# Kernel optimization log

Measured on AMD Instinct MI355X. Metric: run time of the kernel, lower is better.

The kernel has to match this reference:

```python
import jax, jax.numpy as jnp
import numpy as np


def setup_inputs() -> dict:
    key = jax.random.key(0)
    B, L, H, D = 8, 1024, 16, 64
    total_N = B * L
    qkv = jax.random.normal(key, (total_N, 3, H, D), dtype=jnp.float32)
    cu_seqlens = (jnp.arange(B + 1) * L).astype(jnp.int32)  # [B+1] cumulative lengths
    return {"qkv": qkv, "cu_seqlens": cu_seqlens, "max_seqlen": L}


def reference(qkv, cu_seqlens, max_seqlen):
    # qkv: [total_N, 3, H, D]; cu_seqlens: [B+1] int32
    total_N, _, H, D = qkv.shape
    scale = float(D) ** -0.5  # default softmax_scale = 1/sqrt(D)
    q, k, v = qkv[:, 0], qkv[:, 1], qkv[:, 2]  # each [total_N, H, D]

    starts = cu_seqlens[:-1]  # [B]
    ends = cu_seqlens[1:]     # [B]
    # Gather each ragged sequence into a padded [B, L, H, D] layout.
    pos = starts[:, None] + jnp.arange(max_seqlen, dtype=cu_seqlens.dtype)  # [B, L]
    valid = pos < ends[:, None]                                            # [B, L]
    idx = jnp.minimum(pos, total_N - 1)
    qp = q[idx]  # [B, L, H, D]
    kp = k[idx]
    vp = v[idx]

    # Per-sequence non-causal attention, softmax over keys of the same sequence.
    scores = jnp.einsum('bqhd,bkhd->bhqk', qp, kp) * scale  # [B, H, L, L]
    scores = jnp.where(valid[:, None, None, :], scores, jnp.float32(-1e30))
    attn = jax.nn.softmax(scores, axis=-1)
    outp = jnp.einsum('bhqk,bkhd->bqhd', attn, vp)  # [B, L, H, D]
    outp = outp * valid[:, :, None, None].astype(outp.dtype)  # zero padded queries

    # Scatter back to packed layout (invalid slots contribute zeros).
    out = jnp.zeros((total_N, H, D), dtype=qkv.dtype)
    out = out.at[idx.reshape(-1)].add(outp.reshape(-1, H, D))
    return out
```

## Files before the change

kernel.cpp:

```cpp
#include <hip/hip_runtime.h>


typedef __attribute__((ext_vector_type(4))) float f32x4;
typedef __attribute__((ext_vector_type(16))) float f32x16;
typedef __attribute__((ext_vector_type(8))) __bf16 bf16x8;
typedef __attribute__((ext_vector_type(8))) unsigned short us8;

#if __has_builtin(__builtin_amdgcn_exp2f)
#define EXP2F __builtin_amdgcn_exp2f
#else
#define EXP2F exp2f
#endif
#if __has_builtin(__builtin_amdgcn_rcpf)
#define RCPF __builtin_amdgcn_rcpf
#else
#define RCPF(x) (1.0f / (x))
#endif

__device__ __forceinline__ unsigned pk_bf16(float a, float b) {
#if __has_builtin(__builtin_amdgcn_cvt_pk_bf16_f32)
  auto r = __builtin_amdgcn_cvt_pk_bf16_f32(a, b);
  return __builtin_bit_cast(unsigned, r);
#else
  unsigned ra = __builtin_bit_cast(unsigned, a) + 0x8000u;
  unsigned rb = __builtin_bit_cast(unsigned, b) + 0x8000u;
  return __builtin_amdgcn_perm(rb, ra, 0x07060302u);
#endif
}

#define KSTR 72
#define BUFUS (128 * KSTR)
#define KO(b) ((b) * BUFUS)
#define VO(b) ((b) * BUFUS + 64 * KSTR)

#define BAR() asm volatile("s_waitcnt lgkmcnt(0)\n\ts_barrier" ::: "memory")

#define ISSUE(KT)                                                             \
  do {                                                                        \
    const int kb_ = (KT) * 64;                                                \
    int kt_ = s0 + kb_ + krow;                                                \
    kt_ = kt_ > tmax ? tmax : kt_;                                            \
    const float* kp_ = qkv + (size_t)kt_ * 3072 + 1024 + h64 + kd8;           \
    k0 = *(const float4*)kp_;                                                 \
    k1 = *(const float4*)(kp_ + 4);                                           \
    _Pragma("unroll") for (int cc_ = 0; cc_ < 2; ++cc_) {                     \
      _Pragma("unroll") for (int t_ = 0; t_ < 4; ++t_) {                      \
        int vt_ = s0 + kb_ + vk0 + cc_ * 4 + t_;                              \
        vt_ = vt_ > tmax ? tmax : vt_;                                        \
        vv[cc_][t_] = qkv[(size_t)vt_ * 3072 + 2048 + h64 + lane];            \
      }                                                                       \
    }                                                                         \
  } while (0)

#define COMMIT(BI)                                                            \
  do {                                                                        \
    uint4 kw_ = {pk_bf16(k0.x, k0.y), pk_bf16(k0.z, k0.w),                    \
                 pk_bf16(k1.x, k1.y), pk_bf16(k1.z, k1.w)};                   \
    *(uint4*)&smem[KO(BI) + krow * KSTR + kd8] = kw_;                         \
    _Pragma("unroll") for (int cc_ = 0; cc_ < 2; ++cc_) {                     \
      uint2 vw_ = {pk_bf16(vv[cc_][0], vv[cc_][1]),                           \
                   pk_bf16(vv[cc_][2], vv[cc_][3])};                          \
      *(uint2*)&smem[VO(BI) + lane * KSTR + vk0 + cc_ * 4] = vw_;             \
    }                                                                         \
  } while (0)

__launch_bounds__(512, 4)
__global__ void vla_fa_kernel(const float* __restrict__ qkv,
                              const int* __restrict__ cu,
                              float* __restrict__ out,
                              int B, int nflat) {
  __shared__ __align__(16) unsigned short smem[2 * BUFUS];
  __shared__ __align__(16) float ldsL[256];
  const int tid = threadIdx.x;
  const int wave = tid >> 6, lane = tid & 63;
  const int q5 = lane & 31, hi = lane >> 5;
  const int krow = tid >> 3, kd8 = (tid & 7) * 8;
  const int vk0 = wave * 8;
  const int BH = B * 16;

  for (int flat = blockIdx.x; flat < nflat; flat += gridDim.x) {
    const int b = flat % B;
    const int h = (flat / B) & 15;
    const int qb = flat / BH;
    const int s0 = cu[b], s1 = cu[b + 1];
    const int len = s1 - s0;
    if (qb * 256 >= len) continue;
    const int tmax = s1 - 1;
    const int h64 = h * 64;
    const int nkt = (len + 63) >> 6;

    float4 k0, k1;
    float vv[2][4];
    ISSUE(0);

    const float fs = 0.18033688011112042f;
    int qtok = s0 + qb * 256 + wave * 32 + q5;
    qtok = qtok > tmax ? tmax : qtok;
    const float* qp = qkv + (size_t)qtok * 3072 + h64 + hi * 8;
    bf16x8 qf[4];
#pragma unroll
    for (int ks = 0; ks < 4; ++ks) {
      float4 a = *(const float4*)(qp + ks * 16);
      float4 c = *(const float4*)(qp + ks * 16 + 4);
      uint4 w = {pk_bf16(a.x * fs, a.y * fs), pk_bf16(a.z * fs, a.w * fs),
                 pk_bf16(c.x * fs, c.y * fs), pk_bf16(c.z * fs, c.w * fs)};
      qf[ks] = __builtin_bit_cast(bf16x8, w);
    }

    f32x16 Oc[2];
#pragma unroll
    for (int dt = 0; dt < 2; ++dt)
#pragma unroll
      for (int i = 0; i < 16; ++i) Oc[dt][i] = 0.f;
    float lacc[4] = {0.f, 0.f, 0.f, 0.f};

    COMMIT(0);
    if (nkt > 1) ISSUE(1);
    BAR();

    for (int kt = 0; kt < nkt; ++kt) {
      const int cur = kt & 1;
      const int kbase = kt * 64;
      const bool partial = (len - kbase) < 64;
      bf16x8 paf[4];

#pragma unroll
      for (int t = 0; t < 2; ++t) {
        f32x16 S;
#pragma unroll
        for (int i = 0; i < 16; ++i) S[i] = 0.f;
        const int krd = KO(cur) + (t * 32 + q5) * KSTR + hi * 8;
        __builtin_amdgcn_s_setprio(1);
#pragma unroll
        for (int ks = 0; ks < 4; ++ks) {
          bf16x8 kf =
              __builtin_bit_cast(bf16x8, *(const us8*)&smem[krd + ks * 16]);
          S = __builtin_amdgcn_mfma_f32_32x32x16_bf16(kf, qf[ks], S, 0, 0, 0);
        }
        __builtin_amdgcn_s_setprio(0);
        if (partial) {
#pragma unroll
          for (int r = 0; r < 16; ++r) {
            const int key = t * 32 + (r & 3) + ((r >> 2) << 3) + hi * 4;
            if (kbase + key >= len) S[r] = -1e30f;
          }
        }
        float p[16];
#pragma unroll
        for (int r = 0; r < 16; ++r) p[r] = EXP2F(S[r]);
#pragma unroll
        for (int r = 0; r < 16; ++r) lacc[r & 3] += p[r];
#pragma unroll
        for (int m = 0; m < 2; ++m) {
          unsigned w0 = pk_bf16(p[m * 8 + 0], p[m * 8 + 1]);
          unsigned w1 = pk_bf16(p[m * 8 + 2], p[m * 8 + 3]);
          unsigned w2 = pk_bf16(p[m * 8 + 4], p[m * 8 + 5]);
          unsigned w3 = pk_bf16(p[m * 8 + 6], p[m * 8 + 7]);
          asm("v_permlane32_swap_b32 %0, %1" : "+v"(w0), "+v"(w2));
          asm("v_permlane32_swap_b32 %0, %1" : "+v"(w1), "+v"(w3));
          uint4 fw = {w0, w1, w2, w3};
          paf[t * 2 + m] = __builtin_bit_cast(bf16x8, fw);
        }
      }

      if (kt + 1 < nkt) {
        COMMIT(cur ^ 1);
        if (kt + 2 < nkt) ISSUE(kt + 2);
      }

      __builtin_amdgcn_s_setprio(1);
#pragma unroll
      for (int dt = 0; dt < 2; ++dt) {
        const int vrd = VO(cur) + (dt * 32 + q5) * KSTR + hi * 8;
#pragma unroll
        for (int kc = 0; kc < 4; ++kc) {
          bf16x8 vf =
              __builtin_bit_cast(bf16x8, *(const us8*)&smem[vrd + kc * 16]);
          Oc[dt] =
              __builtin_amdgcn_mfma_f32_32x32x16_bf16(paf[kc], vf, Oc[dt], 0, 0, 0);
        }
      }
      __builtin_amdgcn_s_setprio(0);
      BAR();
    }

    float lt = (lacc[0] + lacc[1]) + (lacc[2] + lacc[3]);
    lt += __shfl_xor(lt, 32, 64);
    if (hi == 0) ldsL[wave * 32 + q5] = lt;
    asm volatile("s_waitcnt lgkmcnt(0)" ::: "memory");
    const int rbase = qb * 256 + wave * 32;
#pragma unroll
    for (int g = 0; g < 4; ++g) {
      f32x4 lv = *(const f32x4*)&ldsL[wave * 32 + g * 8 + hi * 4];
#pragma unroll
      for (int j = 0; j < 4; ++j) {
        const int r = g * 4 + j;
        const int row = rbase + g * 8 + hi * 4 + j;
        if (row < len) {
          const float rl = RCPF(lv[j]);
          float* op = out + (size_t)(s0 + row) * 1024 + h64 + q5;
          op[0] = Oc[0][r] * rl;
          op[32] = Oc[1][r] * rl;
        }
      }
    }
  }
}

extern "C" void kernel_launch(void* const* d_in, const int* in_sizes, int n_in,
                              void* d_out, int out_size, void* d_ws, size_t ws_size,
                              hipStream_t stream) {
  const float* qkv = (const float*)d_in[0];
  const int* cu = (const int*)d_in[1];
  float* out = (float*)d_out;
  int B = in_sizes[1] - 1;
  int total_N = in_sizes[0] / (3 * 16 * 64);
  int qbmax = (total_N + 255) / 256;
  int nflat = B * 16 * qbmax;
  int nb = nflat < 512 ? nflat : 512;
  dim3 grid(nb), block(512, 1, 1);
  hipLaunchKernelGGL(vla_fa_kernel, grid, block, 0, stream, qkv, cu, out, B, nflat);
}
```

Baseline: 198.6 us.

## Software-pipeline QK^T of next tile with PV of previous tile

Restructures the key-tile loop so that each iteration issues the QK^T MFMAs for tile kt together with the PV MFMAs for tile kt-1, then does exp/pack afterwards. This lets the matrix cores overlap with the softmax exponent and bf16 packing work. It adds a prologue and epilogue and a triple-buffered V region in shared memory, which raises LDS use and register pressure from holding two score tiles plus the P fragments.

```diff
diff --git a/kernel.cpp b/kernel.cpp
--- a/kernel.cpp
+++ b/kernel.cpp
@@ -29,15 +29,15 @@
 }
 
 #define KSTR 72
-#define BUFUS (128 * KSTR)
-#define KO(b) ((b) * BUFUS)
-#define VO(b) ((b) * BUFUS + 64 * KSTR)
+#define KBUF(b) ((b) * (64 * KSTR))
+#define VBUF(b) ((2 + (b)) * (64 * KSTR))
+#define SMEM_US (5 * 64 * KSTR)
 
 #define BAR() asm volatile("s_waitcnt lgkmcnt(0)\n\ts_barrier" ::: "memory")
 
-#define ISSUE(KT)                                                             \
-  do {                                                                        \
-    const int kb_ = (KT) * 64;                                                \
+#define ISSUE(T)                                                              \
+  do {                                                                        \
+    const int kb_ = (T) * 64;                                                 \
     int kt_ = s0 + kb_ + krow;                                                \
     kt_ = kt_ > tmax ? tmax : kt_;                                            \
     const float* kp_ = qkv + (size_t)kt_ * 3072 + 1024 + h64 + kd8;           \
@@ -52,15 +52,63 @@
     }                                                                         \
   } while (0)
 
-#define COMMIT(BI)                                                            \
-  do {                                                                        \
+#define COMMIT(T)                                                             \
+  do {                                                                        \
+    const int kbi_ = (T) & 1, vbi_ = (T) % 3;                                 \
     uint4 kw_ = {pk_bf16(k0.x, k0.y), pk_bf16(k0.z, k0.w),                    \
                  pk_bf16(k1.x, k1.y), pk_bf16(k1.z, k1.w)};                   \
-    *(uint4*)&smem[KO(BI) + krow * KSTR + kd8] = kw_;                         \
+    *(uint4*)&smem[KBUF(kbi_) + krow * KSTR + kd8] = kw_;                     \
     _Pragma("unroll") for (int cc_ = 0; cc_ < 2; ++cc_) {                     \
       uint2 vw_ = {pk_bf16(vv[cc_][0], vv[cc_][1]),                           \
                    pk_bf16(vv[cc_][2], vv[cc_][3])};                          \
-      *(uint2*)&smem[VO(BI) + lane * KSTR + vk0 + cc_ * 4] = vw_;             \
+      *(uint2*)&smem[VBUF(vbi_) + lane * KSTR + vk0 + cc_ * 4] = vw_;         \
+    }                                                                         \
+  } while (0)
+
+#define QKT(SREG, TT, KB)                                                     \
+  do {                                                                        \
+    const int krd_ = KBUF(KB) + ((TT) * 32 + q5) * KSTR + hi * 8;             \
+    _Pragma("unroll") for (int ks_ = 0; ks_ < 4; ++ks_) {                     \
+      bf16x8 kf_ =                                                            \
+          __builtin_bit_cast(bf16x8, *(const us8*)&smem[krd_ + ks_ * 16]);    \
+      SREG = __builtin_amdgcn_mfma_f32_32x32x16_bf16(kf_, qf[ks_], SREG, 0,   \
+                                                     0, 0);                   \
+    }                                                                         \
+  } while (0)
+
+#define EXPPACK(SREG, TT)                                                     \
+  do {                                                                        \
+    if (partial) {                                                            \
+      _Pragma("unroll") for (int r_ = 0; r_ < 16; ++r_) {                     \
+        const int key_ = (TT) * 32 + (r_ & 3) + ((r_ >> 2) << 3) + hi * 4;    \
+        if (kbase + key_ >= len) SREG[r_] = -1e30f;                           \
+      }                                                                       \
+    }                                                                         \
+    float p_[16];                                                             \
+    _Pragma("unroll") for (int r_ = 0; r_ < 16; ++r_) p_[r_] = EXP2F(SREG[r_]); \
+    _Pragma("unroll") for (int r_ = 0; r_ < 16; ++r_) lacc[r_ & 3] += p_[r_]; \
+    _Pragma("unroll") for (int m_ = 0; m_ < 2; ++m_) {                        \
+      unsigned w0_ = pk_bf16(p_[m_ * 8 + 0], p_[m_ * 8 + 1]);                 \
+      unsigned w1_ = pk_bf16(p_[m_ * 8 + 2], p_[m_ * 8 + 3]);                 \
+      unsigned w2_ = pk_bf16(p_[m_ * 8 + 4], p_[m_ * 8 + 5]);                 \
+      unsigned w3_ = pk_bf16(p_[m_ * 8 + 6], p_[m_ * 8 + 7]);                 \
+      asm("v_permlane32_swap_b32 %0, %1" : "+v"(w0_), "+v"(w2_));             \
+      asm("v_permlane32_swap_b32 %0, %1" : "+v"(w1_), "+v"(w3_));             \
+      uint4 fw_ = {w0_, w1_, w2_, w3_};                                       \
+      paf[(TT) * 2 + m_] = __builtin_bit_cast(bf16x8, fw_);                   \
+    }                                                                         \
+  } while (0)
+
+#define PV(VB)                                                                \
+  do {                                                                        \
+    _Pragma("unroll") for (int dt_ = 0; dt_ < 2; ++dt_) {                     \
+      const int vrd_ = VBUF(VB) + (dt_ * 32 + q5) * KSTR + hi * 8;            \
+      _Pragma("unroll") for (int kc_ = 0; kc_ < 4; ++kc_) {                   \
+        bf16x8 vf_ =                                                          \
+            __builtin_bit_cast(bf16x8, *(const us8*)&smem[vrd_ + kc_ * 16]);  \
+        Oc[dt_] = __builtin_amdgcn_mfma_f32_32x32x16_bf16(paf[kc_], vf_,      \
+                                                          Oc[dt_], 0, 0, 0); \
+      }                                                                       \
     }                                                                         \
   } while (0)
 
@@ -69,7 +117,7 @@
                               const int* __restrict__ cu,
                               float* __restrict__ out,
                               int B, int nflat) {
-  __shared__ __align__(16) unsigned short smem[2 * BUFUS];
+  __shared__ __align__(16) unsigned short smem[SMEM_US];
   __shared__ __align__(16) float ldsL[256];
   const int tid = threadIdx.x;
   const int wave = tid >> 6, lane = tid & 63;
@@ -113,76 +161,56 @@
 #pragma unroll
       for (int i = 0; i < 16; ++i) Oc[dt][i] = 0.f;
     float lacc[4] = {0.f, 0.f, 0.f, 0.f};
-
+    bf16x8 paf[4];
+
+    BAR();
     COMMIT(0);
     if (nkt > 1) ISSUE(1);
     BAR();
 
-    for (int kt = 0; kt < nkt; ++kt) {
-      const int cur = kt & 1;
+    {
+      const int kbase = 0;
+      const bool partial = len < 64;
+      f32x16 S0, S1;
+#pragma unroll
+      for (int i = 0; i < 16; ++i) { S0[i] = 0.f; S1[i] = 0.f; }
+      __builtin_amdgcn_s_setprio(1);
+      QKT(S0, 0, 0);
+      QKT(S1, 1, 0);
+      __builtin_amdgcn_s_setprio(0);
+      if (nkt > 1) COMMIT(1);
+      if (nkt > 2) ISSUE(2);
+      EXPPACK(S0, 0);
+      EXPPACK(S1, 1);
+      BAR();
+    }
+
+    for (int kt = 1; kt < nkt; ++kt) {
       const int kbase = kt * 64;
       const bool partial = (len - kbase) < 64;
-      bf16x8 paf[4];
-
-#pragma unroll
-      for (int t = 0; t < 2; ++t) {
-        f32x16 S;
-#pragma unroll
-        for (int i = 0; i < 16; ++i) S[i] = 0.f;
-        const int krd = KO(cur) + (t * 32 + q5) * KSTR + hi * 8;
-        __builtin_amdgcn_s_setprio(1);
-#pragma unroll
-        for (int ks = 0; ks < 4; ++ks) {
-          bf16x8 kf =
-              __builtin_bit_cast(bf16x8, *(const us8*)&smem[krd + ks * 16]);
-          S = __builtin_amdgcn_mfma_f32_32x32x16_bf16(kf, qf[ks], S, 0, 0, 0);
-        }
-        __builtin_amdgcn_s_setprio(0);
-        if (partial) {
-#pragma unroll
-          for (int r = 0; r < 16; ++r) {
-            const int key = t * 32 + (r & 3) + ((r >> 2) << 3) + hi * 4;
-            if (kbase + key >= len) S[r] = -1e30f;
-          }
-        }
-        float p[16];
-#pragma unroll
-        for (int r = 0; r < 16; ++r) p[r] = EXP2F(S[r]);
-#pragma unroll
-        for (int r = 0; r < 16; ++r) lacc[r & 3] += p[r];
-#pragma unroll
-        for (int m = 0; m < 2; ++m) {
-          unsigned w0 = pk_bf16(p[m * 8 + 0], p[m * 8 + 1]);
-          unsigned w1 = pk_bf16(p[m * 8 + 2], p[m * 8 + 3]);
-          unsigned w2 = pk_bf16(p[m * 8 + 4], p[m * 8 + 5]);
-          unsigned w3 = pk_bf16(p[m * 8 + 6], p[m * 8 + 7]);
-          asm("v_permlane32_swap_b32 %0, %1" : "+v"(w0), "+v"(w2));
-          asm("v_permlane32_swap_b32 %0, %1" : "+v"(w1), "+v"(w3));
-          uint4 fw = {w0, w1, w2, w3};
-          paf[t * 2 + m] = __builtin_bit_cast(bf16x8, fw);
-        }
-      }
-
-      if (kt + 1 < nkt) {
-        COMMIT(cur ^ 1);
-        if (kt + 2 < nkt) ISSUE(kt + 2);
-      }
+      const int kb = kt & 1;
+      const int vbPrev = (kt - 1) % 3;
+      f32x16 S0, S1;
+#pragma unroll
+      for (int i = 0; i < 16; ++i) { S0[i] = 0.f; S1[i] = 0.f; }
 
       __builtin_amdgcn_s_setprio(1);
-#pragma unroll
-      for (int dt = 0; dt < 2; ++dt) {
-        const int vrd = VO(cur) + (dt * 32 + q5) * KSTR + hi * 8;
-#pragma unroll
-        for (int kc = 0; kc < 4; ++kc) {
-          bf16x8 vf =
-              __builtin_bit_cast(bf16x8, *(const us8*)&smem[vrd + kc * 16]);
-          Oc[dt] =
-              __builtin_amdgcn_mfma_f32_32x32x16_bf16(paf[kc], vf, Oc[dt], 0, 0, 0);
-        }
-      }
+      QKT(S0, 0, kb);
+      QKT(S1, 1, kb);
+      PV(vbPrev);
       __builtin_amdgcn_s_setprio(0);
+
+      if (kt + 1 < nkt) COMMIT(kt + 1);
+      if (kt + 2 < nkt) ISSUE(kt + 2);
+
+      EXPPACK(S0, 0);
+      EXPPACK(S1, 1);
       BAR();
     }
+
+    __builtin_amdgcn_s_setprio(1);
+    PV((nkt - 1) % 3);
+    __builtin_amdgcn_s_setprio(0);
 
     float lt = (lacc[0] + lacc[1]) + (lacc[2] + lacc[3]);
     lt += __shfl_xor(lt, 32, 64);
```

Measured after the change: 187.3 us. 5.7% less time.
